# Kernel tuning notes

Hardware: AMD Instinct MI355X
Metric: run time of the kernel (lower is better)

The kernel has to match this reference:

```python
import jax, jax.numpy as jnp
import numpy as np

N_ENT = 40000
D = 128
B = 1024
EPS = 1e-7  # BCE clamp for numerical stability (torch clamps logs internally)


def _cdist_euclidean(a, e):
    # a: [B, D], e: [N, D] -> [B, N] via GEMM-based squared-distance expansion
    sq = jnp.sum(a * a, axis=1)[:, None] + jnp.sum(e * e, axis=1)[None, :] - 2.0 * (a @ e.T)
    return jnp.sqrt(jnp.maximum(sq, 0.0))


def _cdist_manhattan(a, e):
    # Sequential over batch rows to avoid materializing [B, N, D]
    return jax.lax.map(lambda row: jnp.sum(jnp.abs(row[None, :] - e), axis=1), a)


def _branch_loss(c, ent, t_idx, l1_flag, positive):
    dist = _cdist_manhattan(c, ent) if l1_flag else _cdist_euclidean(c, ent)
    # original Python double-loop: dist[i][j] = 1/dist[i][j] * 100
    scaled = 100.0 / jnp.maximum(dist, 1e-12)
    pred = jnp.clip(jax.nn.sigmoid(scaled), EPS, 1.0 - EPS)
    if positive:
        y = jnp.zeros_like(pred).at[jnp.arange(pred.shape[0]), t_idx].set(1.0)
        bce = y * jnp.log(pred) + (1.0 - y) * jnp.log(1.0 - pred)
    else:
        # negative branch writes 0 into an all-zeros target -> y == 0
        bce = jnp.log(1.0 - pred)
    return -jnp.mean(bce)


def setup_inputs() -> dict:
    key = jax.random.key(0)
    ks = jax.random.split(key, 7)
    return {
        "pos_h_batch": jax.random.randint(ks[0], (B,), 0, N_ENT),
        "pos_t_batch": jax.random.randint(ks[1], (B,), 0, N_ENT),
        "neg_h_batch": jax.random.randint(ks[2], (B,), 0, N_ENT),
        "neg_t_batch": jax.random.randint(ks[3], (B,), 0, N_ENT),
        "rseq_pos": jax.random.normal(ks[4], (B, D), jnp.float32),
        "rseq_neg": jax.random.normal(ks[5], (B, D), jnp.float32),
        "ent_embeddings": jax.random.normal(ks[6], (N_ENT, D), jnp.float32),
        "L1_flag": 0,
    }


def reference(pos_h_batch, pos_t_batch, neg_h_batch, neg_t_batch, rseq_pos, rseq_neg, ent_embeddings, L1_flag):
    l1 = bool(L1_flag)
    # positive branch
    c_t_pos = ent_embeddings[pos_h_batch] + rseq_pos
    loss1 = _branch_loss(c_t_pos, ent_embeddings, pos_t_batch, l1, positive=True)
    # negative branch (neg_t_batch only feeds an unused c_h_e in the original)
    c_t_neg = ent_embeddings[neg_h_batch] + rseq_neg
    loss2 = _branch_loss(c_t_neg, ent_embeddings, None, l1, positive=False)
    return loss1 + loss2
```

## Files before the change

### kernel.cpp

```cpp
#include <hip/hip_runtime.h>
#include <cstdint>
#include <cstddef>

#define N_ENT 40000
#define DDIM  128
#define BSZ   1024
#define NJT   313
#define NPART (16 * NJT)
#define NGRID 5120

#define AS1 __attribute__((address_space(1)))
#define AS3 __attribute__((address_space(3)))

typedef short s16x8 __attribute__((ext_vector_type(8)));
typedef float f32x4 __attribute__((ext_vector_type(4)));

#define OFF_PART  0
#define OFF_TPART 20480
#define OFF_ENORM 24576
#define OFF_CNORM 184576
#define OFF_CBF   192768
#define OFF_EBF   717056

#define S_CLAMP 15.9423847f
#define U_CLAMP 0.159423847f
#define LP_MAX (-1.1920929e-7f)

__device__ __forceinline__ unsigned short f2bf(float f) {
  uint32_t u = __float_as_uint(f);
  u += 0x7fffu + ((u >> 16) & 1u);
  return (unsigned short)(u >> 16);
}

__global__ __launch_bounds__(256) void prep_k(const float* __restrict__ ent,
                                              const int* __restrict__ pos_h,
                                              const int* __restrict__ pos_t,
                                              const int* __restrict__ neg_h,
                                              const float* __restrict__ rpos,
                                              const float* __restrict__ rneg,
                                              const int* __restrict__ l1_flag,
                                              unsigned short* __restrict__ ent_bf,
                                              float* __restrict__ enorm,
                                              unsigned short* __restrict__ c_bf,
                                              float* __restrict__ cnorm,
                                              float* __restrict__ tpart) {
  const int lane = threadIdx.x & 63, wv = threadIdx.x >> 6;
  const int ih = lane >> 5, il = lane & 31;
  const int blk = blockIdx.x;
  if (blk < 5000) {
    int row = blk * 8 + wv * 2 + ih;
    float4 v = reinterpret_cast<const float4*>(ent + (size_t)row * DDIM)[il];
    ushort4 h4; h4.x = f2bf(v.x); h4.y = f2bf(v.y); h4.z = f2bf(v.z); h4.w = f2bf(v.w);
    reinterpret_cast<ushort4*>(ent_bf + (size_t)row * DDIM)[il] = h4;
    float sq = fmaf(v.x, v.x, fmaf(v.y, v.y, fmaf(v.z, v.z, v.w * v.w)));
    #pragma unroll
    for (int m = 1; m <= 16; m <<= 1) sq += __shfl_xor(sq, m);
    if (il == 0) enorm[row] = sq;
  } else {
    int row = (blk - 5000) * 8 + wv * 2 + ih;
    int br = row >> 10, i = row & 1023;
    int h = br ? neg_h[i] : pos_h[i];
    const float* rs = br ? rneg : rpos;
    float4 e  = reinterpret_cast<const float4*>(ent + (size_t)h * DDIM)[il];
    float4 rv = reinterpret_cast<const float4*>(rs + (size_t)i * DDIM)[il];
    float c0 = e.x + rv.x, c1 = e.y + rv.y, c2 = e.z + rv.z, c3 = e.w + rv.w;
    ushort4 h4; h4.x = f2bf(c0); h4.y = f2bf(c1); h4.z = f2bf(c2); h4.w = f2bf(c3);
    reinterpret_cast<ushort4*>(c_bf + (size_t)row * DDIM)[il] = h4;
    float sq = fmaf(c0, c0, fmaf(c1, c1, fmaf(c2, c2, c3 * c3)));
    #pragma unroll
    for (int m = 1; m <= 16; m <<= 1) sq += __shfl_xor(sq, m);
    if (il == 0) cnorm[row] = sq;
    if (br == 0) {
      int t = pos_t[i];
      float4 et = reinterpret_cast<const float4*>(ent + (size_t)t * DDIM)[il];
      float d0 = c0 - et.x, d1 = c1 - et.y, d2v = c2 - et.z, d3 = c3 - et.w;
      float d2 = fmaf(d0, d0, fmaf(d1, d1, fmaf(d2v, d2v, d3 * d3)));
      float m1 = fabsf(d0) + fabsf(d1) + fabsf(d2v) + fabsf(d3);
      #pragma unroll
      for (int m = 1; m <= 16; m <<= 1) { d2 += __shfl_xor(d2, m); m1 += __shfl_xor(m1, m); }
      if (il == 0) {
        float s = (*l1_flag) ? (100.f / fmaxf(m1, 1e-12f))
                             : (100.f * rsqrtf(fmaxf(d2, 0.f)));
        float x  = __expf(-s);
        float L  = log1pf(x);
        float Bt = fminf(-L, LP_MAX);
        float Ap = fmaxf(-s, -S_CLAMP);
        tpart[i] = Bt - Ap;
      }
    }
  }
}

__global__ __launch_bounds__(256) void main_k(const unsigned short* __restrict__ c_bf,
                                              const unsigned short* __restrict__ ent_bf,
                                              const float* __restrict__ cnorm,
                                              const float* __restrict__ enorm,
                                              const int* __restrict__ l1_flag,
                                              const int* __restrict__ pos_h,
                                              const int* __restrict__ neg_h,
                                              const float* __restrict__ rpos,
                                              const float* __restrict__ rneg,
                                              const float* __restrict__ ent_f32,
                                              float* __restrict__ partials) {
  __shared__ unsigned short smem[128 * 128];
  const int id = blockIdx.x;
  const int c8 = id & 7;
  const int q  = id >> 3;
  const int tg = q >> 4;
  const int mm = q & 15;
  const int jt = c8 + tg * 8;
  if (jt >= NJT) return;
  const int branch = mm & 1;
  const int it = mm >> 1;
  const int i0 = it * 128, j0 = jt * 128;
  const int tid = threadIdx.x, lane = tid & 63, wv = tid >> 6;
  const int wm = wv >> 1, wn = wv & 1;
  const int r15 = lane & 15, quad = lane >> 4;

  #pragma unroll
  for (int i = 0; i < 8; ++i) {
    int g  = i * 256 + tid;
    int r  = g >> 4;
    int cp = g & 15;
    int c  = cp ^ (r & 15);
    int jr = j0 + r; if (jr >= N_ENT) jr = N_ENT - 1;
    const unsigned short* src = ent_bf + (size_t)jr * DDIM + c * 8;
    __builtin_amdgcn_global_load_lds((const AS1 void*)src, (AS3 void*)(&smem[g * 8]), 16, 0, 0);
  }

  const unsigned short* Abase = c_bf + ((size_t)(branch << 10) + i0) * DDIM;
  const unsigned short* arow[4];
  #pragma unroll
  for (int tm = 0; tm < 4; ++tm)
    arow[tm] = Abase + (size_t)(wm * 64 + tm * 16 + r15) * DDIM + quad * 8;

  s16x8 av[2][4];
  #pragma unroll
  for (int tm = 0; tm < 4; ++tm)
    av[0][tm] = *reinterpret_cast<const s16x8*>(arow[tm]);

  float en[4];
  #pragma unroll
  for (int tn = 0; tn < 4; ++tn) {
    int jg = j0 + wn * 64 + tn * 16 + r15;
    en[tn] = enorm[jg < N_ENT ? jg : N_ENT - 1];
  }
  float cnv[16];
  #pragma unroll
  for (int tm = 0; tm < 4; ++tm)
    #pragma unroll
    for (int r = 0; r < 4; ++r)
      cnv[tm * 4 + r] = cnorm[(branch << 10) + i0 + wm * 64 + tm * 16 + quad * 4 + r];

  f32x4 acc[4][4];
  const f32x4 zf = {0.f, 0.f, 0.f, 0.f};
  #pragma unroll
  for (int a = 0; a < 4; ++a)
    #pragma unroll
    for (int b = 0; b < 4; ++b) acc[a][b] = zf;

  __syncthreads();

  #pragma unroll
  for (int kc = 0; kc < 4; ++kc) {
    if (kc < 3) {
      #pragma unroll
      for (int tm = 0; tm < 4; ++tm)
        av[(kc + 1) & 1][tm] = *reinterpret_cast<const s16x8*>(arow[tm] + (kc + 1) * 32);
    }
    s16x8 bv[4];
    #pragma unroll
    for (int tn = 0; tn < 4; ++tn) {
      int R  = wn * 64 + tn * 16 + r15;
      int cs = (kc * 4 + quad) ^ r15;
      bv[tn] = *reinterpret_cast<const s16x8*>(&smem[R * 128 + cs * 8]);
    }
    #pragma unroll
    for (int tm = 0; tm < 4; ++tm)
      #pragma unroll
      for (int tn = 0; tn < 4; ++tn)
        acc[tm][tn] = __builtin_amdgcn_mfma_f32_16x16x32_bf16(av[kc & 1][tm], bv[tn], acc[tm][tn], 0, 0, 0);
  }

  const int l1 = *l1_flag;
  float lsum = 0.f;
  const bool full = (j0 + 128) <= N_ENT;

  if (!l1) {
    #pragma unroll
    for (int tm = 0; tm < 4; ++tm) {
      if (full) {
        #pragma unroll
        for (int tn = 0; tn < 4; ++tn) {
          float e0 = en[tn];
          #pragma unroll
          for (int r = 0; r < 4; ++r) {
            float u = rsqrtf(fmaf(-2.f, acc[tm][tn][r], cnv[tm * 4 + r] + e0));
            lsum += fminf(u, U_CLAMP);
          }
        }
      } else {
        #pragma unroll
        for (int tn = 0; tn < 4; ++tn) {
          int jg = j0 + wn * 64 + tn * 16 + r15;
          if (jg < N_ENT) {
            float e0 = en[tn];
            #pragma unroll
            for (int r = 0; r < 4; ++r) {
              float u = rsqrtf(fmaf(-2.f, acc[tm][tn][r], cnv[tm * 4 + r] + e0));
              lsum += fminf(u, U_CLAMP);
            }
          }
        }
      }
    }
  } else {
    const float* rs = branch ? rneg : rpos;
    const int*   hb = branch ? neg_h : pos_h;
    #pragma unroll 1
    for (int tm = 0; tm < 4; ++tm) {
      #pragma unroll 1
      for (int r = 0; r < 4; ++r) {
        int bi = i0 + wm * 64 + tm * 16 + quad * 4 + r;
        int h  = hb[bi];
        #pragma unroll 1
        for (int tn = 0; tn < 4; ++tn) {
          int jg = j0 + wn * 64 + tn * 16 + r15;
          if (jg < N_ENT) {
            const float* cp1 = ent_f32 + (size_t)h * DDIM;
            const float* cp2 = rs + (size_t)bi * DDIM;
            const float* ep  = ent_f32 + (size_t)jg * DDIM;
            float man = 0.f;
            #pragma unroll 1
            for (int d = 0; d < DDIM; ++d) man += fabsf(cp1[d] + cp2[d] - ep[d]);
            float s = 100.f / fmaxf(man, 1e-12f);
            lsum += 0.01f * fminf(s, S_CLAMP);
          }
        }
      }
    }
  }

  #pragma unroll
  for (int m = 32; m; m >>= 1) lsum += __shfl_xor(lsum, m);
  __shared__ float s4[4];
  if (lane == 0) s4[wv] = lsum;
  __syncthreads();
  if (tid == 0)
    partials[jt * 16 + mm] = s4[0] + s4[1] + s4[2] + s4[3];
}

__global__ __launch_bounds__(256) void finalize_k(const float* __restrict__ partials,
                                                  const float* __restrict__ tpart,
                                                  float* __restrict__ out) {
  const int b = blockIdx.x, tid = threadIdx.x, lane = tid & 63, wv = tid >> 6;
  const double inv = 1.0 / ((double)BSZ * (double)N_ENT);
  double v = 0.0;
  if (b < 20) {
    int i = b * 256 + tid;
    if (i < NPART) v = (double)partials[i] * (100.0 * inv);
  } else {
    int i = (b - 20) * 256 + tid;
    v = (double)tpart[i] * (-inv);
  }
  #pragma unroll
  for (int m = 32; m; m >>= 1) v += __shfl_xor(v, m);
  __shared__ double sd[4];
  if (lane == 0) sd[wv] = v;
  __syncthreads();
  if (tid == 0) atomicAdd(out, (float)(sd[0] + sd[1] + sd[2] + sd[3]));
}

extern "C" void kernel_launch(void* const* d_in, const int* in_sizes, int n_in,
                              void* d_out, int out_size, void* d_ws, size_t ws_size,
                              hipStream_t stream) {
  const int*   pos_h = (const int*)d_in[0];
  const int*   pos_t = (const int*)d_in[1];
  const int*   neg_h = (const int*)d_in[2];
  const float* rpos  = (const float*)d_in[4];
  const float* rneg  = (const float*)d_in[5];
  const float* ent   = (const float*)d_in[6];
  const int*   l1    = (const int*)d_in[7];

  char* ws = (char*)d_ws;
  float*          partials = (float*)(ws + OFF_PART);
  float*          tpart    = (float*)(ws + OFF_TPART);
  float*          enorm    = (float*)(ws + OFF_ENORM);
  float*          cnorm    = (float*)(ws + OFF_CNORM);
  unsigned short* c_bf     = (unsigned short*)(ws + OFF_CBF);
  unsigned short* ent_bf   = (unsigned short*)(ws + OFF_EBF);

  hipMemsetAsync(d_out, 0, sizeof(float), stream);

  prep_k<<<5256, 256, 0, stream>>>(ent, pos_h, pos_t, neg_h, rpos, rneg, l1,
                                   ent_bf, enorm, c_bf, cnorm, tpart);

  main_k<<<NGRID, 256, 0, stream>>>(c_bf, ent_bf, cnorm, enorm, l1,
                                    pos_h, neg_h, rpos, rneg, ent, partials);

  finalize_k<<<24, 256, 0, stream>>>(partials, tpart, (float*)d_out);
}
```

Baseline: 145.8 us.

## Fuse entity bf16 conversion and norm computation into the GEMM tile loader

The prep pass that converted the whole entity table to bf16 and computed its squared norms is removed. The main kernel now loads fp32 entity rows directly, computes the row norms with shuffles into shared memory, and packs them to bf16 by truncation before storing to LDS. This drops a full write and reread of the bf16 table plus one kernel's worth of work. In exchange, each entity tile is loaded as fp32 (twice the bytes) by every block that uses it, uses truncation instead of round-to-nearest, and replaces the async global-to-LDS load with register staging.

```diff
diff --git a/kernel.cpp b/kernel.cpp
--- a/kernel.cpp
+++ b/kernel.cpp
@@ -9,18 +9,13 @@
 #define NPART (16 * NJT)
 #define NGRID 5120
 
-#define AS1 __attribute__((address_space(1)))
-#define AS3 __attribute__((address_space(3)))
-
 typedef short s16x8 __attribute__((ext_vector_type(8)));
 typedef float f32x4 __attribute__((ext_vector_type(4)));
 
 #define OFF_PART  0
 #define OFF_TPART 20480
-#define OFF_ENORM 24576
-#define OFF_CNORM 184576
-#define OFF_CBF   192768
-#define OFF_EBF   717056
+#define OFF_CNORM 24576
+#define OFF_CBF   32768
 
 #define S_CLAMP 15.9423847f
 #define U_CLAMP 0.159423847f
@@ -39,70 +34,55 @@
                                               const float* __restrict__ rpos,
                                               const float* __restrict__ rneg,
                                               const int* __restrict__ l1_flag,
-                                              unsigned short* __restrict__ ent_bf,
-                                              float* __restrict__ enorm,
                                               unsigned short* __restrict__ c_bf,
                                               float* __restrict__ cnorm,
                                               float* __restrict__ tpart) {
   const int lane = threadIdx.x & 63, wv = threadIdx.x >> 6;
   const int ih = lane >> 5, il = lane & 31;
-  const int blk = blockIdx.x;
-  if (blk < 5000) {
-    int row = blk * 8 + wv * 2 + ih;
-    float4 v = reinterpret_cast<const float4*>(ent + (size_t)row * DDIM)[il];
-    ushort4 h4; h4.x = f2bf(v.x); h4.y = f2bf(v.y); h4.z = f2bf(v.z); h4.w = f2bf(v.w);
-    reinterpret_cast<ushort4*>(ent_bf + (size_t)row * DDIM)[il] = h4;
-    float sq = fmaf(v.x, v.x, fmaf(v.y, v.y, fmaf(v.z, v.z, v.w * v.w)));
-    #pragma unroll
-    for (int m = 1; m <= 16; m <<= 1) sq += __shfl_xor(sq, m);
-    if (il == 0) enorm[row] = sq;
-  } else {
-    int row = (blk - 5000) * 8 + wv * 2 + ih;
-    int br = row >> 10, i = row & 1023;
-    int h = br ? neg_h[i] : pos_h[i];
-    const float* rs = br ? rneg : rpos;
-    float4 e  = reinterpret_cast<const float4*>(ent + (size_t)h * DDIM)[il];
-    float4 rv = reinterpret_cast<const float4*>(rs + (size_t)i * DDIM)[il];
-    float c0 = e.x + rv.x, c1 = e.y + rv.y, c2 = e.z + rv.z, c3 = e.w + rv.w;
-    ushort4 h4; h4.x = f2bf(c0); h4.y = f2bf(c1); h4.z = f2bf(c2); h4.w = f2bf(c3);
-    reinterpret_cast<ushort4*>(c_bf + (size_t)row * DDIM)[il] = h4;
-    float sq = fmaf(c0, c0, fmaf(c1, c1, fmaf(c2, c2, c3 * c3)));
-    #pragma unroll
-    for (int m = 1; m <= 16; m <<= 1) sq += __shfl_xor(sq, m);
-    if (il == 0) cnorm[row] = sq;
-    if (br == 0) {
-      int t = pos_t[i];
-      float4 et = reinterpret_cast<const float4*>(ent + (size_t)t * DDIM)[il];
-      float d0 = c0 - et.x, d1 = c1 - et.y, d2v = c2 - et.z, d3 = c3 - et.w;
-      float d2 = fmaf(d0, d0, fmaf(d1, d1, fmaf(d2v, d2v, d3 * d3)));
-      float m1 = fabsf(d0) + fabsf(d1) + fabsf(d2v) + fabsf(d3);
-      #pragma unroll
-      for (int m = 1; m <= 16; m <<= 1) { d2 += __shfl_xor(d2, m); m1 += __shfl_xor(m1, m); }
-      if (il == 0) {
-        float s = (*l1_flag) ? (100.f / fmaxf(m1, 1e-12f))
-                             : (100.f * rsqrtf(fmaxf(d2, 0.f)));
-        float x  = __expf(-s);
-        float L  = log1pf(x);
-        float Bt = fminf(-L, LP_MAX);
-        float Ap = fmaxf(-s, -S_CLAMP);
-        tpart[i] = Bt - Ap;
-      }
+  int row = blockIdx.x * 8 + wv * 2 + ih;
+  int br = row >> 10, i = row & 1023;
+  int h = br ? neg_h[i] : pos_h[i];
+  const float* rs = br ? rneg : rpos;
+  float4 e  = reinterpret_cast<const float4*>(ent + (size_t)h * DDIM)[il];
+  float4 rv = reinterpret_cast<const float4*>(rs + (size_t)i * DDIM)[il];
+  float c0 = e.x + rv.x, c1 = e.y + rv.y, c2 = e.z + rv.z, c3 = e.w + rv.w;
+  ushort4 h4; h4.x = f2bf(c0); h4.y = f2bf(c1); h4.z = f2bf(c2); h4.w = f2bf(c3);
+  reinterpret_cast<ushort4*>(c_bf + (size_t)row * DDIM)[il] = h4;
+  float sq = fmaf(c0, c0, fmaf(c1, c1, fmaf(c2, c2, c3 * c3)));
+  #pragma unroll
+  for (int m = 1; m <= 16; m <<= 1) sq += __shfl_xor(sq, m);
+  if (il == 0) cnorm[row] = sq;
+  if (br == 0) {
+    int t = pos_t[i];
+    float4 et = reinterpret_cast<const float4*>(ent + (size_t)t * DDIM)[il];
+    float d0 = c0 - et.x, d1 = c1 - et.y, d2v = c2 - et.z, d3 = c3 - et.w;
+    float d2 = fmaf(d0, d0, fmaf(d1, d1, fmaf(d2v, d2v, d3 * d3)));
+    float m1 = fabsf(d0) + fabsf(d1) + fabsf(d2v) + fabsf(d3);
+    #pragma unroll
+    for (int m = 1; m <= 16; m <<= 1) { d2 += __shfl_xor(d2, m); m1 += __shfl_xor(m1, m); }
+    if (il == 0) {
+      float s = (*l1_flag) ? (100.f / fmaxf(m1, 1e-12f))
+                           : (100.f * rsqrtf(fmaxf(d2, 0.f)));
+      float x  = __expf(-s);
+      float L  = log1pf(x);
+      float Bt = fminf(-L, LP_MAX);
+      float Ap = fmaxf(-s, -S_CLAMP);
+      tpart[i] = Bt - Ap;
     }
   }
 }
 
 __global__ __launch_bounds__(256) void main_k(const unsigned short* __restrict__ c_bf,
-                                              const unsigned short* __restrict__ ent_bf,
+                                              const float* __restrict__ ent_f32,
                                               const float* __restrict__ cnorm,
-                                              const float* __restrict__ enorm,
                                               const int* __restrict__ l1_flag,
                                               const int* __restrict__ pos_h,
                                               const int* __restrict__ neg_h,
                                               const float* __restrict__ rpos,
                                               const float* __restrict__ rneg,
-                                              const float* __restrict__ ent_f32,
                                               float* __restrict__ partials) {
   __shared__ unsigned short smem[128 * 128];
+  __shared__ float rn[128];
   const int id = blockIdx.x;
   const int c8 = id & 7;
   const int q  = id >> 3;
@@ -124,8 +104,20 @@
     int cp = g & 15;
     int c  = cp ^ (r & 15);
     int jr = j0 + r; if (jr >= N_ENT) jr = N_ENT - 1;
-    const unsigned short* src = ent_bf + (size_t)jr * DDIM + c * 8;
-    __builtin_amdgcn_global_load_lds((const AS1 void*)src, (AS3 void*)(&smem[g * 8]), 16, 0, 0);
+    const float4* src = reinterpret_cast<const float4*>(ent_f32 + (size_t)jr * DDIM + c * 8);
+    float4 v0 = src[0], v1 = src[1];
+    float sq = fmaf(v0.x, v0.x, fmaf(v0.y, v0.y, fmaf(v0.z, v0.z,
+               fmaf(v0.w, v0.w, fmaf(v1.x, v1.x, fmaf(v1.y, v1.y,
+               fmaf(v1.z, v1.z, v1.w * v1.w)))))));
+    #pragma unroll
+    for (int m = 1; m <= 8; m <<= 1) sq += __shfl_xor(sq, m);
+    if ((lane & 15) == 0) rn[r] = sq;
+    uint32_t w0 = (__float_as_uint(v0.x) >> 16) | (__float_as_uint(v0.y) & 0xffff0000u);
+    uint32_t w1 = (__float_as_uint(v0.z) >> 16) | (__float_as_uint(v0.w) & 0xffff0000u);
+    uint32_t w2 = (__float_as_uint(v1.x) >> 16) | (__float_as_uint(v1.y) & 0xffff0000u);
+    uint32_t w3 = (__float_as_uint(v1.z) >> 16) | (__float_as_uint(v1.w) & 0xffff0000u);
+    int4 pk; pk.x = (int)w0; pk.y = (int)w1; pk.z = (int)w2; pk.w = (int)w3;
+    *reinterpret_cast<int4*>(&smem[g * 8]) = pk;
   }
 
   const unsigned short* Abase = c_bf + ((size_t)(branch << 10) + i0) * DDIM;
@@ -139,12 +131,6 @@
   for (int tm = 0; tm < 4; ++tm)
     av[0][tm] = *reinterpret_cast<const s16x8*>(arow[tm]);
 
-  float en[4];
-  #pragma unroll
-  for (int tn = 0; tn < 4; ++tn) {
-    int jg = j0 + wn * 64 + tn * 16 + r15;
-    en[tn] = enorm[jg < N_ENT ? jg : N_ENT - 1];
-  }
   float cnv[16];
   #pragma unroll
   for (int tm = 0; tm < 4; ++tm)
@@ -160,6 +146,11 @@
     for (int b = 0; b < 4; ++b) acc[a][b] = zf;
 
   __syncthreads();
+
+  float en[4];
+  #pragma unroll
+  for (int tn = 0; tn < 4; ++tn)
+    en[tn] = rn[wn * 64 + tn * 16 + r15];
 
   #pragma unroll
   for (int kc = 0; kc < 4; ++kc) {
@@ -285,18 +276,16 @@
   char* ws = (char*)d_ws;
   float*          partials = (float*)(ws + OFF_PART);
   float*          tpart    = (float*)(ws + OFF_TPART);
-  float*          enorm    = (float*)(ws + OFF_ENORM);
   float*          cnorm    = (float*)(ws + OFF_CNORM);
   unsigned short* c_bf     = (unsigned short*)(ws + OFF_CBF);
-  unsigned short* ent_bf   = (unsigned short*)(ws + OFF_EBF);
 
   hipMemsetAsync(d_out, 0, sizeof(float), stream);
 
-  prep_k<<<5256, 256, 0, stream>>>(ent, pos_h, pos_t, neg_h, rpos, rneg, l1,
-                                   ent_bf, enorm, c_bf, cnorm, tpart);
-
-  main_k<<<NGRID, 256, 0, stream>>>(c_bf, ent_bf, cnorm, enorm, l1,
-                                    pos_h, neg_h, rpos, rneg, ent, partials);
+  prep_k<<<256, 256, 0, stream>>>(ent, pos_h, pos_t, neg_h, rpos, rneg, l1,
+                                  c_bf, cnorm, tpart);
+
+  main_k<<<NGRID, 256, 0, stream>>>(c_bf, ent, cnorm, l1,
+                                    pos_h, neg_h, rpos, rneg, partials);
 
   finalize_k<<<24, 256, 0, stream>>>(partials, tpart, (float*)d_out);
 }
```

New measurement: 154.9 us. 1.06x slower.
